# Kernel tuning notes

Measured on AMD Instinct MI355X. Metric: run time of the kernel, lower is better.

Reference implementation:

```python
import jax, jax.numpy as jnp
import numpy as np

EMBED_DIM = 1024
NUM_HEADS = 16
HEAD_DIM = EMBED_DIM // NUM_HEADS
NEG = -1000000000.0


def setup_inputs() -> dict:
    key = jax.random.key(0)
    ks = jax.random.split(key, 13)
    B, S, D = 4, 2048, EMBED_DIM
    scale = 1.0 / np.sqrt(D)
    inp = {
        "query": jax.random.normal(ks[0], (B, S, D), jnp.float32),
        "key": jax.random.normal(ks[1], (B, S, D), jnp.float32),
        "value": jax.random.normal(ks[2], (B, S, D), jnp.float32),
        "mask": jax.random.randint(ks[3], (B, 1, 1, S), 0, 2, jnp.int32),
        "Wq": jax.random.normal(ks[4], (D, D), jnp.float32) * scale,
        "bq": jnp.zeros((D,), jnp.float32),
        "Wk": jax.random.normal(ks[5], (D, D), jnp.float32) * scale,
        "bk": jnp.zeros((D,), jnp.float32),
        "Wv": jax.random.normal(ks[6], (D, D), jnp.float32) * scale,
        "bv": jnp.zeros((D,), jnp.float32),
        "Wo": jax.random.normal(ks[7], (D, D), jnp.float32) * scale,
        "bo": jnp.zeros((D,), jnp.float32),
    }
    return inp


def _split_heads(x):
    B, S, D = x.shape
    return x.reshape(B, S, NUM_HEADS, HEAD_DIM).transpose(0, 2, 1, 3)  # [B,H,S,hd]


def reference(query, key, value, mask, Wq, bq, Wk, bk, Wv, bv, Wo, bo):
    B, S, D = query.shape
    Q = _split_heads(query @ Wq + bq)
    K = _split_heads(key @ Wk + bk)
    V = _split_heads(value @ Wv + bv)
    scores = jnp.einsum("bhqd,bhkd->bhqk", Q, K) / jnp.sqrt(jnp.float32(HEAD_DIM))
    scores = jnp.where(mask == 0, jnp.float32(NEG), scores)
    attn = jax.nn.softmax(scores, axis=-1)
    out = jnp.einsum("bhqk,bhkd->bhqd", attn, V)
    out = out.transpose(0, 2, 1, 3).reshape(B, S, D)
    return out @ Wo + bo
```

## Files before the change

### kernel.cpp

```cpp
#include <hip/hip_runtime.h>


#define SEQ   2048
#define EDIM  1024
#define NHEAD 16
#define HDIM  64
#define NBAT  4
#define MTOK  8192

typedef __attribute__((ext_vector_type(8))) __bf16 bf16x8;
typedef __attribute__((ext_vector_type(4))) __bf16 bf16x4;
typedef __attribute__((ext_vector_type(4))) float f32x4;
typedef __attribute__((ext_vector_type(16))) float f32x16;
typedef __attribute__((ext_vector_type(8))) unsigned short us8;
typedef unsigned short u16;

#define SCL   0.1803368801111244f

__device__ __forceinline__ u16 bfbits(float f) {
    __bf16 h = (__bf16)f;
    return __builtin_bit_cast(u16, h);
}
__device__ __forceinline__ bf16x8 bc(us8 v) { return __builtin_bit_cast(bf16x8, v); }
__device__ __forceinline__ float exp2fast(float x) {
    float r;
    asm("v_exp_f32 %0, %1" : "=v"(r) : "v"(x));
    return r;
}
__device__ __forceinline__ void glds16(const void* g, void* l) {
    __builtin_amdgcn_global_load_lds(
        (const __attribute__((address_space(1))) unsigned int*)g,
        (__attribute__((address_space(3))) unsigned int*)l, 16, 0, 0);
}

__global__ __launch_bounds__(256) void prep_kernel(const int* __restrict__ mask,
                                                   int* __restrict__ idxl,
                                                   int* __restrict__ cntp) {
    __shared__ int psum[257];
    const int b = blockIdx.x, t = threadIdx.x;
    const int* mp = mask + b * SEQ;
    int m8[8]; int s = 0;
#pragma unroll
    for (int i = 0; i < 8; ++i) { m8[i] = mp[t * 8 + i]; s += (m8[i] != 0); }
    psum[t + 1] = s;
    __syncthreads();
    if (t == 0) { psum[0] = 0; for (int i = 1; i <= 256; ++i) psum[i] += psum[i - 1]; }
    __syncthreads();
    int ex = psum[t];
#pragma unroll
    for (int i = 0; i < 8; ++i)
        if (m8[i] != 0) idxl[b * SEQ + (ex++)] = t * 8 + i;
    if (t == 0) cntp[b] = psum[256];
}

__global__ __launch_bounds__(256) void wtrans4_kernel(const float* __restrict__ W0,
                                                      const float* __restrict__ W1,
                                                      const float* __restrict__ W2,
                                                      const float* __restrict__ W3,
                                                      u16* __restrict__ WT) {
    __shared__ float tile[32][33];
    const int tx = threadIdx.x, ty = threadIdx.y;
    const int bx = blockIdx.x,  by = blockIdx.y, wz = blockIdx.z;
    const float* W = (wz == 0) ? W0 : (wz == 1) ? W1 : (wz == 2) ? W2 : W3;
    u16* O = WT + (size_t)wz * EDIM * EDIM;
#pragma unroll
    for (int i = 0; i < 4; ++i)
        tile[ty + i * 8][tx] = W[(size_t)(by * 32 + ty + i * 8) * EDIM + bx * 32 + tx];
    __syncthreads();
#pragma unroll
    for (int i = 0; i < 4; ++i) {
        int n = bx * 32 + ty + i * 8;
        int k = by * 32 + tx;
        O[(size_t)n * EDIM + k] = bfbits(tile[tx][ty + i * 8]);
    }
}

__global__ __launch_bounds__(256) void cvt3_kernel(const float* __restrict__ q,
                                                   const float* __restrict__ k,
                                                   const float* __restrict__ v,
                                                   u16* __restrict__ oq,
                                                   u16* __restrict__ ok,
                                                   u16* __restrict__ ov) {
    const int sel = blockIdx.y;
    const float* a = (sel == 0) ? q : (sel == 1) ? k : v;
    u16* o = (sel == 0) ? oq : (sel == 1) ? ok : ov;
    const size_t i = ((size_t)blockIdx.x * 256 + threadIdx.x) * 8;
    f32x4 v0 = *(const f32x4*)(a + i);
    f32x4 v1 = *(const f32x4*)(a + i + 4);
    us8 r;
#pragma unroll
    for (int j = 0; j < 4; ++j) { r[j] = bfbits(v0[j]); r[4 + j] = bfbits(v1[j]); }
    *(us8*)(o + i) = r;
}

template <bool ABF16>
__global__ __launch_bounds__(256) void qkv_gemm_kernel(
        const void* __restrict__ Aq, const void* __restrict__ Ak,
        const void* __restrict__ Av, const u16* __restrict__ WTall,
        const float* __restrict__ bqp, const float* __restrict__ bkp,
        const float* __restrict__ bvp,
        u16* __restrict__ Qb, u16* __restrict__ Kb, u16* __restrict__ Vb,
        const int* __restrict__ idxl, const int* __restrict__ cntp) {
    const int id    = blockIdx.x;
    const int which = id >> 9;
    const int sub   = id & 511;
    const int r_    = sub >> 3;
    const int grp   = r_ >> 5, bnq = (r_ >> 2) & 7, bmin = r_ & 3;
    const int bm    = (sub & 7) + 8 * (grp * 4 + bmin);
    const int bn    = bnq;

    const void*  A    = (which == 0) ? Aq : (which == 1) ? Ak : Av;
    const u16*   WT   = WTall + (size_t)which * EDIM * EDIM;
    const float* bias = (which == 0) ? bqp : (which == 1) ? bkp : bvp;
    u16*         outp = (which == 0) ? Qb : (which == 1) ? Kb : Vb;
    const float  oscale = (which == 1) ? SCL : 1.0f;
    const bool   gather = (which > 0);

    int cn = SEQ;
    if (gather) {
        cn = cntp[bm >> 4];
        if (((bm & 15) * 128) >= cn) return;
    }

    __shared__ __align__(16) char Asraw[2][128 * 32 * (ABF16 ? 2 : 4)];
    __shared__ __align__(16) u16  Bs[2][128][32];

    const int tid  = threadIdx.x;
    const int lane = tid & 63, w = tid >> 6;
    const int g    = lane >> 4, l15 = lane & 15;
    const int wrow = w >> 1, wcol = w & 1;

    const char* pa[ABF16 ? 2 : 4];
    if constexpr (ABF16) {
        const u16* Ab = (const u16*)A;
#pragma unroll
        for (int t = 0; t < 2; ++t) {
            const int rloc = w * 32 + t * 16 + (lane >> 2);
            int arow;
            if (gather) {
                const int sloc = (bm & 15) * 128 + rloc;
                const int gi = (sloc < cn) ? idxl[(bm >> 4) * SEQ + sloc] : 0;
                arow = (bm >> 4) * SEQ + gi;
            } else arow = bm * 128 + rloc;
            const int scol = ((lane & 3) ^ ((lane >> 3) & 3)) * 8;
            pa[t] = (const char*)(Ab + (size_t)arow * EDIM + scol);
        }
    } else {
        const float* Af = (const float*)A;
#pragma unroll
        for (int t = 0; t < 4; ++t) {
            const int rloc = w * 32 + t * 8 + (lane >> 3);
            int arow;
            if (gather) {
                const int sloc = (bm & 15) * 128 + rloc;
                const int gi = (sloc < cn) ? idxl[(bm >> 4) * SEQ + sloc] : 0;
                arow = (bm >> 4) * SEQ + gi;
            } else arow = bm * 128 + rloc;
            const int scol = ((lane & 7) ^ (lane >> 3)) * 4;
            pa[t] = (const char*)(Af + (size_t)arow * EDIM + scol);
        }
    }
    const char* pb[2];
#pragma unroll
    for (int t = 0; t < 2; ++t) {
        const int rloc = w * 32 + t * 16 + (lane >> 2);
        const int brow = bn * 128 + rloc;
        const int scol = ((lane & 3) ^ ((lane >> 3) & 3)) * 8;
        pb[t] = (const char*)(WT + (size_t)brow * EDIM + scol);
    }

    auto STAGE = [&](int bufn, int ko) {
        char* abase = &Asraw[bufn][0] + w * (ABF16 ? 2048 : 4096);
        if constexpr (ABF16) {
#pragma unroll
            for (int t = 0; t < 2; ++t)
                glds16(pa[t] + (size_t)ko * 2, abase + t * 1024);
        } else {
#pragma unroll
            for (int t = 0; t < 4; ++t)
                glds16(pa[t] + (size_t)ko * 4, abase + t * 1024);
        }
        char* bbase = (char*)&Bs[bufn][0][0] + w * 2048;
#pragma unroll
        for (int t = 0; t < 2; ++t)
            glds16(pb[t] + (size_t)ko * 2, bbase + t * 1024);
    };

    f32x4 acc[4][4] = {};
    constexpr int NT = EDIM / 32;

    STAGE(0, 0);
    __syncthreads();

    int buf = 0;
#pragma unroll 1
    for (int kt = 0; kt < NT; ++kt) {
        if (kt < NT - 1) STAGE(buf ^ 1, (kt + 1) * 32);

        bf16x8 af[4], bfr[4];
        if constexpr (ABF16) {
            const u16* As = (const u16*)&Asraw[buf][0];
            const int x = (l15 >> 1) & 3;
#pragma unroll
            for (int i = 0; i < 4; ++i) {
                const int row = wrow * 64 + i * 16 + l15;
                af[i] = bc(*(const us8*)(As + row * 32 + ((g ^ x) * 8)));
            }
        } else {
            const float* As = (const float*)&Asraw[buf][0];
            const int x = l15 & 7;
#pragma unroll
            for (int i = 0; i < 4; ++i) {
                const int row = wrow * 64 + i * 16 + l15;
                f32x4 u0 = *(const f32x4*)(As + row * 32 + (((2 * g)     ^ x) * 4));
                f32x4 u1 = *(const f32x4*)(As + row * 32 + (((2 * g + 1) ^ x) * 4));
#pragma unroll
                for (int j = 0; j < 4; ++j) {
                    af[i][j]     = (__bf16)u0[j];
                    af[i][4 + j] = (__bf16)u1[j];
                }
            }
        }
        {
            const int x = (l15 >> 1) & 3;
#pragma unroll
            for (int j = 0; j < 4; ++j) {
                const int row = wcol * 64 + j * 16 + l15;
                bfr[j] = bc(*(const us8*)((const u16*)&Bs[buf][0][0] + row * 32 + ((g ^ x) * 8)));
            }
        }

#pragma unroll
        for (int i = 0; i < 4; ++i)
#pragma unroll
            for (int j = 0; j < 4; ++j)
                acc[i][j] = __builtin_amdgcn_mfma_f32_16x16x32_bf16(af[i], bfr[j], acc[i][j], 0, 0, 0);

        __syncthreads();
        buf ^= 1;
    }

#pragma unroll
    for (int i = 0; i < 4; ++i) {
#pragma unroll
        for (int j = 0; j < 4; ++j) {
            const int gm0 = bm * 128 + wrow * 64 + i * 16 + g * 4;
            const int gn  = bn * 128 + wcol * 64 + j * 16 + l15;
            const float bv = bias[gn];
#pragma unroll
            for (int r = 0; r < 4; ++r) {
                float val = (acc[i][j][r] + bv) * oscale;
                const int m = gm0 + r;
                if (gather && (m & 2047) >= cn) val = 0.f;
                const int b = m >> 11, s = m & 2047;
                const int h = gn >> 6, d = gn & 63;
                if (which == 2)
                    outp[((size_t)(b * NHEAD + h) << 17) + d * SEQ + s] = bfbits(val);
                else
                    outp[((size_t)(b * NHEAD + h) << 17) + s * HDIM + d] = bfbits(val);
            }
        }
    }
}

__global__ __launch_bounds__(256) void o_gemm_kernel(const u16* __restrict__ Ap,
                                                     const u16* __restrict__ WT,
                                                     const float* __restrict__ bias,
                                                     float* __restrict__ outp) {
    const int id  = blockIdx.x;
    const int r_  = id >> 3;
    const int grp = r_ >> 5, bnq = (r_ >> 2) & 7, bmin = r_ & 3;
    const int bm  = (id & 7) + 8 * (grp * 4 + bmin);
    const int bn  = bnq;

    __shared__ __align__(16) u16 As[2][128][32];
    __shared__ __align__(16) u16 Bs[2][128][32];

    const int tid  = threadIdx.x;
    const int lane = tid & 63, w = tid >> 6;
    const int g    = lane >> 4, l15 = lane & 15;
    const int wrow = w >> 1, wcol = w & 1;

    const char* pa[2]; const char* pb[2];
#pragma unroll
    for (int t = 0; t < 2; ++t) {
        const int rloc = w * 32 + t * 16 + (lane >> 2);
        const int scol = ((lane & 3) ^ ((lane >> 3) & 3)) * 8;
        pa[t] = (const char*)(Ap + (size_t)(bm * 128 + rloc) * EDIM + scol);
        pb[t] = (const char*)(WT + (size_t)(bn * 128 + rloc) * EDIM + scol);
    }

    auto STAGE = [&](int bufn, int ko) {
        char* abase = (char*)&As[bufn][0][0] + w * 2048;
        char* bbase = (char*)&Bs[bufn][0][0] + w * 2048;
#pragma unroll
        for (int t = 0; t < 2; ++t) {
            glds16(pa[t] + (size_t)ko * 2, abase + t * 1024);
            glds16(pb[t] + (size_t)ko * 2, bbase + t * 1024);
        }
    };

    f32x4 acc[4][4] = {};
    constexpr int NT = EDIM / 32;

    STAGE(0, 0);
    __syncthreads();

    int buf = 0;
#pragma unroll 1
    for (int kt = 0; kt < NT; ++kt) {
        if (kt < NT - 1) STAGE(buf ^ 1, (kt + 1) * 32);

        bf16x8 af[4], bfr[4];
        const int x = (l15 >> 1) & 3;
#pragma unroll
        for (int i = 0; i < 4; ++i) {
            const int rowA = wrow * 64 + i * 16 + l15;
            af[i] = bc(*(const us8*)((const u16*)&As[buf][0][0] + rowA * 32 + ((g ^ x) * 8)));
            const int rowB = wcol * 64 + i * 16 + l15;
            bfr[i] = bc(*(const us8*)((const u16*)&Bs[buf][0][0] + rowB * 32 + ((g ^ x) * 8)));
        }

#pragma unroll
        for (int i = 0; i < 4; ++i)
#pragma unroll
            for (int j = 0; j < 4; ++j)
                acc[i][j] = __builtin_amdgcn_mfma_f32_16x16x32_bf16(af[i], bfr[j], acc[i][j], 0, 0, 0);

        __syncthreads();
        buf ^= 1;
    }

#pragma unroll
    for (int i = 0; i < 4; ++i) {
#pragma unroll
        for (int j = 0; j < 4; ++j) {
            const int gm0 = bm * 128 + wrow * 64 + i * 16 + g * 4;
            const int gn  = bn * 128 + wcol * 64 + j * 16 + l15;
            const float bv = bias[gn];
#pragma unroll
            for (int r = 0; r < 4; ++r)
                outp[(size_t)(gm0 + r) * EDIM + gn] = acc[i][j][r] + bv;
        }
    }
}

__global__ __launch_bounds__(256) void attn_kernel(const u16* __restrict__ Q,
                                                   const u16* __restrict__ K,
                                                   const u16* __restrict__ VT,
                                                   const int* __restrict__ cntp,
                                                   u16* __restrict__ O) {
    __shared__ u16 Klds[2][64][64];
    __shared__ u16 Vlds[2][64][64];

    const int tid = threadIdx.x, lane = tid & 63, w = tid >> 6;
    const int h = lane >> 5, l31 = lane & 31;

    const int id  = blockIdx.x;
    const int bh  = (id & 7) * 8 + ((id >> 3) >> 4);
    const int qb  = (id >> 3) & 15;
    const int b   = bh >> 4, hd_ = bh & 15;

    const u16* Qp = Q + ((size_t)bh << 17);
    const u16* Kp = K + ((size_t)bh << 17);
    const u16* Vp = VT + ((size_t)bh << 17);
    const int q0w = qb * 128 + w * 32;

    const int cn  = cntp[b];
    const int ktc = (cn + 63) >> 6;

    bf16x8 qf[4];
#pragma unroll
    for (int khd = 0; khd < 4; ++khd)
        qf[khd] = bc(*(const us8*)&Qp[(size_t)(q0w + l31) * HDIM + khd * 16 + h * 8]);

    const int b_  = l31 & 3, hp = (l31 >> 2) & 1, cc = l31 >> 3;
    const int piR = 16 * (cc & 1) + 8 * hp + 4 * (cc >> 1) + b_;
    const int swk = b_ | (hp << 2);
    const int swv = l31 & 7;

    const int lr = lane >> 3, lg = lane & 7;
    const u16* pKs[2]; const u16* pVs[2];
#pragma unroll
    for (int t = 0; t < 2; ++t) {
        const int rloc = w * 16 + t * 8 + lr;
        const int xk = (rloc & 3) | (((rloc >> 3) & 1) << 2);
        pKs[t] = Kp + (size_t)rloc * HDIM + ((lg ^ xk) << 3);
        const int xv = rloc & 7;
        pVs[t] = Vp + (size_t)rloc * SEQ + ((lg ^ xv) << 3);
    }

    auto STAGE = [&](int bufn, int kb) {
#pragma unroll
        for (int t = 0; t < 2; ++t) {
            glds16(pKs[t] + (size_t)kb * HDIM, &Klds[bufn][w * 16 + t * 8][0]);
            glds16(pVs[t] + kb,                &Vlds[bufn][w * 16 + t * 8][0]);
        }
    };

    f32x16 ot[2] = {};
    f32x16 ls = {};

    bf16x8 onesf;
#pragma unroll
    for (int j = 0; j < 8; ++j) onesf[j] = (__bf16)1.0f;

    STAGE(0, 0);
    __syncthreads();

    for (int kt = 0; kt < ktc; ++kt) {
        const int cur = kt & 1;
        const bool more = (kt + 1) < ktc;
        if (more) STAGE(cur ^ 1, (kt + 1) * 64);

        f32x16 st[2] = {};
        __builtin_amdgcn_s_setprio(1);
#pragma unroll
        for (int kb2 = 0; kb2 < 2; ++kb2) {
            const u16* Kr = &Klds[cur][kb2 * 32 + piR][0];
#pragma unroll
            for (int khd = 0; khd < 4; ++khd) {
                bf16x8 kf = bc(*(const us8*)&Kr[(khd * 16 + h * 8) ^ (swk << 3)]);
                st[kb2] = __builtin_amdgcn_mfma_f32_32x32x16_bf16(kf, qf[khd], st[kb2], 0, 0, 0);
            }
        }
        __builtin_amdgcn_s_setprio(0);

#pragma unroll
        for (int kb2 = 0; kb2 < 2; ++kb2)
#pragma unroll
            for (int e = 0; e < 16; ++e)
                st[kb2][e] = exp2fast(st[kb2][e]);

        if (kt == ktc - 1) {
            const int kbase = kt * 64;
#pragma unroll
            for (int kb2 = 0; kb2 < 2; ++kb2)
#pragma unroll
                for (int cp = 0; cp < 4; ++cp)
#pragma unroll
                    for (int j = 0; j < 4; ++j) {
                        const int key = kbase + kb2 * 32 + 16 * (cp & 1) + 4 * (cp >> 1) + 8 * h + j;
                        if (key >= cn) st[kb2][cp * 4 + j] = 0.f;
                    }
        }

        bf16x8 pf[4];
#pragma unroll
        for (int s = 0; s < 4; ++s) {
            const int kb2 = s >> 1, sel = (s & 1) * 4;
#pragma unroll
            for (int j = 0; j < 4; ++j) {
                pf[s][j]     = (__bf16)st[kb2][sel + j];
                pf[s][4 + j] = (__bf16)st[kb2][8 + sel + j];
            }
        }

        __builtin_amdgcn_s_setprio(1);
#pragma unroll
        for (int s = 0; s < 4; ++s)
            ls = __builtin_amdgcn_mfma_f32_32x32x16_bf16(onesf, pf[s], ls, 0, 0, 0);
#pragma unroll
        for (int dblk = 0; dblk < 2; ++dblk) {
            const u16* Vr = &Vlds[cur][dblk * 32 + l31][0];
#pragma unroll
            for (int s = 0; s < 4; ++s) {
                bf16x8 vf = bc(*(const us8*)&Vr[(s * 16 + h * 8) ^ (swv << 3)]);
                ot[dblk] = __builtin_amdgcn_mfma_f32_32x32x16_bf16(vf, pf[s], ot[dblk], 0, 0, 0);
            }
        }
        __builtin_amdgcn_s_setprio(0);

        __syncthreads();
    }

    const float inv = 1.f / ls[0];

    const size_t row = (size_t)(b * SEQ + q0w + l31) * EDIM + hd_ * HDIM;
#pragma unroll
    for (int dblk = 0; dblk < 2; ++dblk) {
#pragma unroll
        for (int cp = 0; cp < 4; ++cp) {
            bf16x4 t;
#pragma unroll
            for (int j = 0; j < 4; ++j)
                t[j] = (__bf16)(ot[dblk][cp * 4 + j] * inv);
            *(bf16x4*)&O[row + dblk * 32 + 8 * cp + 4 * h] = t;
        }
    }
}

extern "C" void kernel_launch(void* const* d_in, const int* in_sizes, int n_in,
                              void* d_out, int out_size, void* d_ws, size_t ws_size,
                              hipStream_t stream) {
    const float* query = (const float*)d_in[0];
    const float* key   = (const float*)d_in[1];
    const float* value = (const float*)d_in[2];
    const int*   mask  = (const int*)d_in[3];
    const float* Wq = (const float*)d_in[4];  const float* bq = (const float*)d_in[5];
    const float* Wk = (const float*)d_in[6];  const float* bk = (const float*)d_in[7];
    const float* Wv = (const float*)d_in[8];  const float* bv = (const float*)d_in[9];
    const float* Wo = (const float*)d_in[10]; const float* bo = (const float*)d_in[11];

    char* ws = (char*)d_ws;
    const size_t WT_BYTES  = (size_t)EDIM * EDIM * 2;
    const size_t BUF_BYTES = (size_t)MTOK * EDIM * 2;
    u16* wtq   = (u16*)(ws);
    u16* wto   = (u16*)(ws + 3 * WT_BYTES);
    u16* Qbuf  = (u16*)(ws + 4 * WT_BYTES);
    u16* Kbuf  = (u16*)(ws + 4 * WT_BYTES + BUF_BYTES);
    u16* VTbuf = (u16*)(ws + 4 * WT_BYTES + 2 * BUF_BYTES);
    char* X    = ws + 4 * WT_BYTES + 3 * BUF_BYTES;
    u16* Abuf  = (u16*)X;

    const size_t need_big = 4 * WT_BYTES + 6 * BUF_BYTES + (size_t)MTOK * 4 + 64;
    const bool big = (ws_size >= need_big);
    u16* Abfq = (u16*)X;
    u16* Abfk = (u16*)(X + BUF_BYTES);
    u16* Abfv = (u16*)(X + 2 * BUF_BYTES);
    char* tail = big ? (X + 3 * BUF_BYTES) : (X + BUF_BYTES);
    int* idxl  = (int*)tail;
    int* cntp  = (int*)(tail + (size_t)MTOK * 4);

    prep_kernel<<<NBAT, 256, 0, stream>>>(mask, idxl, cntp);

    dim3 tgrid(32, 32, 4), tblk(32, 8);
    wtrans4_kernel<<<tgrid, tblk, 0, stream>>>(Wq, Wk, Wv, Wo, wtq);

    if (big) {
        cvt3_kernel<<<dim3(4096, 3), 256, 0, stream>>>(query, key, value,
                                                       Abfq, Abfk, Abfv);
        qkv_gemm_kernel<true><<<1536, 256, 0, stream>>>(Abfq, Abfk, Abfv, wtq,
                                                        bq, bk, bv,
                                                        Qbuf, Kbuf, VTbuf,
                                                        idxl, cntp);
    } else {
        qkv_gemm_kernel<false><<<1536, 256, 0, stream>>>(query, key, value, wtq,
                                                         bq, bk, bv,
                                                         Qbuf, Kbuf, VTbuf,
                                                         idxl, cntp);
    }

    attn_kernel<<<1024, 256, 0, stream>>>(Qbuf, Kbuf, VTbuf, cntp, Abuf);

    o_gemm_kernel<<<512, 256, 0, stream>>>(Abuf, wto, bo, (float*)d_out);
}
```

Measured before the change: 186.5 us.

## Triple-buffer GEMM K-loop with partial vmcnt waits and grid-stride bf16 conversion

Both the QKV and output-projection GEMMs move from double to triple buffering in shared memory. Tiles are prefetched two steps ahead, and the full __syncthreads is replaced by s_waitcnt vmcnt(N) plus a raw s_barrier, so only the oldest stage's loads must land before compute. This hides more global-load latency but uses 50% more LDS per block, which may lower occupancy. The fp32-to-bf16 conversion kernel also becomes a grid-stride loop handling 16 elements per thread with a quarter of the blocks.

```diff
diff --git a/kernel.cpp b/kernel.cpp
--- a/kernel.cpp
+++ b/kernel.cpp
@@ -32,6 +32,7 @@
         (const __attribute__((address_space(1))) unsigned int*)g,
         (__attribute__((address_space(3))) unsigned int*)l, 16, 0, 0);
 }
+#define VMCNT(n) asm volatile("s_waitcnt vmcnt(" #n ")" ::: "memory")
 
 __global__ __launch_bounds__(256) void prep_kernel(const int* __restrict__ mask,
                                                    int* __restrict__ idxl,
@@ -84,13 +85,22 @@
     const int sel = blockIdx.y;
     const float* a = (sel == 0) ? q : (sel == 1) ? k : v;
     u16* o = (sel == 0) ? oq : (sel == 1) ? ok : ov;
-    const size_t i = ((size_t)blockIdx.x * 256 + threadIdx.x) * 8;
-    f32x4 v0 = *(const f32x4*)(a + i);
-    f32x4 v1 = *(const f32x4*)(a + i + 4);
-    us8 r;
-#pragma unroll
-    for (int j = 0; j < 4; ++j) { r[j] = bfbits(v0[j]); r[4 + j] = bfbits(v1[j]); }
-    *(us8*)(o + i) = r;
+    const size_t N = (size_t)MTOK * EDIM;
+    const size_t stride = (size_t)gridDim.x * 256 * 16;
+    for (size_t i = ((size_t)blockIdx.x * 256 + threadIdx.x) * 16; i < N; i += stride) {
+        f32x4 v0 = *(const f32x4*)(a + i);
+        f32x4 v1 = *(const f32x4*)(a + i + 4);
+        f32x4 v2 = *(const f32x4*)(a + i + 8);
+        f32x4 v3 = *(const f32x4*)(a + i + 12);
+        us8 r0, r1;
+#pragma unroll
+        for (int j = 0; j < 4; ++j) {
+            r0[j] = bfbits(v0[j]); r0[4 + j] = bfbits(v1[j]);
+            r1[j] = bfbits(v2[j]); r1[4 + j] = bfbits(v3[j]);
+        }
+        *(us8*)(o + i) = r0;
+        *(us8*)(o + i + 8) = r1;
+    }
 }
 
 template <bool ABF16>
@@ -122,8 +132,8 @@
         if (((bm & 15) * 128) >= cn) return;
     }
 
-    __shared__ __align__(16) char Asraw[2][128 * 32 * (ABF16 ? 2 : 4)];
-    __shared__ __align__(16) u16  Bs[2][128][32];
+    __shared__ __align__(16) char Asraw[3][128 * 32 * (ABF16 ? 2 : 4)];
+    __shared__ __align__(16) u16  Bs[3][128][32];
 
     const int tid  = threadIdx.x;
     const int lane = tid & 63, w = tid >> 6;
@@ -190,16 +200,18 @@
     constexpr int NT = EDIM / 32;
 
     STAGE(0, 0);
-    __syncthreads();
-
-    int buf = 0;
+    STAGE(1, 32);
+    if constexpr (ABF16) VMCNT(4); else VMCNT(6);
+    __builtin_amdgcn_s_barrier();
+
+    int bcur = 0, bn1 = 1, bn2 = 2;
 #pragma unroll 1
     for (int kt = 0; kt < NT; ++kt) {
-        if (kt < NT - 1) STAGE(buf ^ 1, (kt + 1) * 32);
+        if (kt + 2 < NT) STAGE(bn2, (kt + 2) * 32);
 
         bf16x8 af[4], bfr[4];
         if constexpr (ABF16) {
-            const u16* As = (const u16*)&Asraw[buf][0];
+            const u16* As = (const u16*)&Asraw[bcur][0];
             const int x = (l15 >> 1) & 3;
 #pragma unroll
             for (int i = 0; i < 4; ++i) {
@@ -207,7 +219,7 @@
                 af[i] = bc(*(const us8*)(As + row * 32 + ((g ^ x) * 8)));
             }
         } else {
-            const float* As = (const float*)&Asraw[buf][0];
+            const float* As = (const float*)&Asraw[bcur][0];
             const int x = l15 & 7;
 #pragma unroll
             for (int i = 0; i < 4; ++i) {
@@ -226,7 +238,7 @@
 #pragma unroll
             for (int j = 0; j < 4; ++j) {
                 const int row = wcol * 64 + j * 16 + l15;
-                bfr[j] = bc(*(const us8*)((const u16*)&Bs[buf][0][0] + row * 32 + ((g ^ x) * 8)));
+                bfr[j] = bc(*(const us8*)((const u16*)&Bs[bcur][0][0] + row * 32 + ((g ^ x) * 8)));
             }
         }
 
@@ -236,8 +248,15 @@
             for (int j = 0; j < 4; ++j)
                 acc[i][j] = __builtin_amdgcn_mfma_f32_16x16x32_bf16(af[i], bfr[j], acc[i][j], 0, 0, 0);
 
-        __syncthreads();
-        buf ^= 1;
+        if (kt + 1 < NT) {
+            if (kt + 2 < NT) {
+                if constexpr (ABF16) VMCNT(4); else VMCNT(6);
+            } else {
+                VMCNT(0);
+            }
+            __builtin_amdgcn_s_barrier();
+        }
+        const int t = bcur; bcur = bn1; bn1 = bn2; bn2 = t;
     }
 
 #pragma unroll
@@ -273,8 +292,8 @@
     const int bm  = (id & 7) + 8 * (grp * 4 + bmin);
     const int bn  = bnq;
 
-    __shared__ __align__(16) u16 As[2][128][32];
-    __shared__ __align__(16) u16 Bs[2][128][32];
+    __shared__ __align__(16) u16 As[3][128][32];
+    __shared__ __align__(16) u16 Bs[3][128][32];
 
     const int tid  = threadIdx.x;
     const int lane = tid & 63, w = tid >> 6;
@@ -304,21 +323,23 @@
     constexpr int NT = EDIM / 32;
 
     STAGE(0, 0);
-    __syncthreads();
-
-    int buf = 0;
+    STAGE(1, 32);
+    VMCNT(4);
+    __builtin_amdgcn_s_barrier();
+
+    int bcur = 0, bn1 = 1, bn2 = 2;
 #pragma unroll 1
     for (int kt = 0; kt < NT; ++kt) {
-        if (kt < NT - 1) STAGE(buf ^ 1, (kt + 1) * 32);
+        if (kt + 2 < NT) STAGE(bn2, (kt + 2) * 32);
 
         bf16x8 af[4], bfr[4];
         const int x = (l15 >> 1) & 3;
 #pragma unroll
         for (int i = 0; i < 4; ++i) {
             const int rowA = wrow * 64 + i * 16 + l15;
-            af[i] = bc(*(const us8*)((const u16*)&As[buf][0][0] + rowA * 32 + ((g ^ x) * 8)));
+            af[i] = bc(*(const us8*)((const u16*)&As[bcur][0][0] + rowA * 32 + ((g ^ x) * 8)));
             const int rowB = wcol * 64 + i * 16 + l15;
-            bfr[i] = bc(*(const us8*)((const u16*)&Bs[buf][0][0] + rowB * 32 + ((g ^ x) * 8)));
+            bfr[i] = bc(*(const us8*)((const u16*)&Bs[bcur][0][0] + rowB * 32 + ((g ^ x) * 8)));
         }
 
 #pragma unroll
@@ -327,8 +348,11 @@
             for (int j = 0; j < 4; ++j)
                 acc[i][j] = __builtin_amdgcn_mfma_f32_16x16x32_bf16(af[i], bfr[j], acc[i][j], 0, 0, 0);
 
-        __syncthreads();
-        buf ^= 1;
+        if (kt + 1 < NT) {
+            if (kt + 2 < NT) { VMCNT(4); } else { VMCNT(0); }
+            __builtin_amdgcn_s_barrier();
+        }
+        const int t = bcur; bcur = bn1; bn1 = bn2; bn2 = t;
     }
 
 #pragma unroll
@@ -528,7 +552,7 @@
     wtrans4_kernel<<<tgrid, tblk, 0, stream>>>(Wq, Wk, Wv, Wo, wtq);
 
     if (big) {
-        cvt3_kernel<<<dim3(4096, 3), 256, 0, stream>>>(query, key, value,
+        cvt3_kernel<<<dim3(1024, 3), 256, 0, stream>>>(query, key, value,
                                                        Abfq, Abfk, Abfv);
         qkv_gemm_kernel<true><<<1536, 256, 0, stream>>>(Abfq, Abfk, Abfv, wtq,
                                                         bq, bk, bv,
```

Result: slower. 194.6 us (+4.3%).
